# Kernel optimization log

Hardware: AMD Instinct MI355X
Metric: run time of the kernel (lower is better)

## Reference

```python
import jax, jax.numpy as jnp
import numpy as np

N, E, G = 4096, 16384, 128   # nodes, edges, graphs
IN, H, ED = 64, 64, 16       # in_dim, hidden, edge_dim


def _lin(key, fan_in, fan_out):
    return jax.random.normal(key, (fan_in, fan_out), dtype=jnp.float32) * (fan_in ** -0.5)


def setup_inputs() -> dict:
    key = jax.random.key(0)
    ks = jax.random.split(key, 32)
    inp = {
        "x": jax.random.normal(ks[0], (N, IN), dtype=jnp.float32),
        "edge_index": jax.random.randint(ks[1], (2, E), 0, N, dtype=jnp.int32),
        "edge_attr": jax.random.normal(ks[2], (E, ED), dtype=jnp.float32),
        "batch": jnp.sort(jax.random.randint(ks[3], (N,), 0, G, dtype=jnp.int32)),
    }
    ki = 4
    dims = [(IN, H), (H, H), (H, H)]  # (in_channels, out_channels) per layer
    for l, (ic, oc) in enumerate(dims):
        hd = ic * oc  # edge-MLP width = hidden * in_channels
        inp[f"l{l}_w1"] = _lin(ks[ki], ED, hd); ki += 1
        inp[f"l{l}_b1"] = jnp.zeros((hd,), dtype=jnp.float32)
        inp[f"l{l}_w2"] = _lin(ks[ki], hd, hd); ki += 1
        inp[f"l{l}_b2"] = jnp.zeros((hd,), dtype=jnp.float32)
        inp[f"l{l}_root"] = _lin(ks[ki], ic, oc); ki += 1
        inp[f"l{l}_bias"] = jnp.zeros((oc,), dtype=jnp.float32)
    return inp


def _nnconv(x, src, dst, edge_attr, w1, b1, w2, b2, root, bias, ic, oc):
    # per-edge weight matrix Theta(e): [E, ic, oc]
    h = jax.nn.relu(edge_attr @ w1 + b1)
    theta = (h @ w2 + b2).reshape(-1, ic, oc)
    # gather source features, per-edge bmm, scatter-mean to target
    msg = jnp.einsum("ei,eio->eo", x[src], theta)
    agg = jax.ops.segment_sum(msg, dst, num_segments=N)
    cnt = jax.ops.segment_sum(jnp.ones((msg.shape[0],), msg.dtype), dst, num_segments=N)
    agg = agg / jnp.maximum(cnt, 1.0)[:, None]
    return agg + x @ root + bias


def reference(x, edge_index, edge_attr, batch,
              l0_w1, l0_b1, l0_w2, l0_b2, l0_root, l0_bias,
              l1_w1, l1_b1, l1_w2, l1_b2, l1_root, l1_bias,
              l2_w1, l2_b1, l2_w2, l2_b2, l2_root, l2_bias):
    src, dst = edge_index[0], edge_index[1]
    layers = [
        (l0_w1, l0_b1, l0_w2, l0_b2, l0_root, l0_bias, IN, H),
        (l1_w1, l1_b1, l1_w2, l1_b2, l1_root, l1_bias, H, H),
        (l2_w1, l2_b1, l2_w2, l2_b2, l2_root, l2_bias, H, H),
    ]
    h = x
    for (w1, b1, w2, b2, root, bias, ic, oc) in layers:
        h = jax.nn.relu(_nnconv(h, src, dst, edge_attr, w1, b1, w2, b2, root, bias, ic, oc))
        # dropout is identity in eval mode
    # global mean pool over graphs
    s = jax.ops.segment_sum(h, batch, num_segments=G)
    c = jax.ops.segment_sum(jnp.ones((N,), h.dtype), batch, num_segments=G)
    return s / jnp.maximum(c, 1.0)[:, None]
```

## Files before the change

kernel.cpp:

```cpp
#include <hip/hip_runtime.h>
#include <hip/hip_bf16.h>

#define NN 4096
#define EE 16384
#define GG 128
#define EDIM 16
#define HD 4096

#define NGROUPS 64
#define GK 8
#define KSUBS 64
#define MAXT 40
#define MAXSLOT (MAXT * 16)
#define MAXTW 5
#define SYHALF (64 * 64 * 8)
#define PANEL (8 * 64 * 64)

typedef __attribute__((ext_vector_type(8))) short short8;
typedef __attribute__((ext_vector_type(4))) float float4v;

static __device__ inline unsigned short f2b(float f) {
    unsigned u = __float_as_uint(f);
    unsigned r = u + 0x7fff + ((u >> 16) & 1);
    return (unsigned short)(r >> 16);
}

static __device__ inline unsigned pk2(float a, float b) {
    __hip_bfloat162 p = __float22bfloat162_rn(make_float2(a, b));
    return *(unsigned*)&p;
}

__global__ void hker(const float* __restrict__ ea, const float* __restrict__ w1,
                     const float* __restrict__ b1, unsigned short* __restrict__ hB) {
    __shared__ float sea[16 * 16];
    const int tid = threadIdx.x;
    const int j = blockIdx.x * 256 + tid;
    const int e0 = blockIdx.y * 16;
    float w[16];
#pragma unroll
    for (int k = 0; k < 16; ++k) w[k] = w1[k * HD + j];
    const float b = b1[j];
    sea[tid] = ea[e0 * EDIM + tid];
    __syncthreads();
#pragma unroll 4
    for (int el = 0; el < 16; ++el) {
        float a = b;
#pragma unroll
        for (int k = 0; k < 16; ++k) a += sea[el * 16 + k] * w[k];
        hB[(size_t)(e0 + el) * HD + j] = f2b(fmaxf(a, 0.f));
    }
}

__global__ void wperm(const float* __restrict__ w2, unsigned short* __restrict__ W2q) {
    __shared__ float t[64 * 65];
    const int k = blockIdx.x;
    const int tid = threadIdx.x;
    const int o = tid & 63, r4 = tid >> 6;
#pragma unroll
    for (int it = 0; it < 16; ++it) {
        int i = it * 4 + r4;
        t[i * 65 + o] = w2[(size_t)k * HD + i * 64 + o];
    }
    __syncthreads();
    const int o2 = tid >> 2, q = tid & 3;
    const int q2 = q >> 1;
    const int j0 = (o2 >> 4) * 2 + q2;
    const int lmm = o2 & 15;
    const int blk = k;
#pragma unroll
    for (int cc = 0; cc < 2; ++cc) {
        const int quad = (q & 1) * 2 + cc;
        const int ib = q * 16 + cc * 8;
        size_t base = ((size_t)(blk * 64 + quad * 16 + lmm)) * 64 + j0 * 8;
        unsigned b0 = pk2(t[(ib + 0) * 65 + o2], t[(ib + 1) * 65 + o2]);
        unsigned b1 = pk2(t[(ib + 2) * 65 + o2], t[(ib + 3) * 65 + o2]);
        unsigned b2_ = pk2(t[(ib + 4) * 65 + o2], t[(ib + 5) * 65 + o2]);
        unsigned b3 = pk2(t[(ib + 6) * 65 + o2], t[(ib + 7) * 65 + o2]);
        *(uint4*)(&W2q[base]) = make_uint4(b0, b1, b2_, b3);
    }
}

__global__ void count_edges(const int* __restrict__ src, const int* __restrict__ dst,
                            int* __restrict__ cnt_src, float* __restrict__ cnt_dst) {
    const int e = blockIdx.x * 256 + threadIdx.x;
    atomicAdd(&cnt_src[src[e]], 1);
    atomicAdd(&cnt_dst[dst[e]], 1.f);
}

__global__ void build_layout(const int* __restrict__ cnt_src, int* __restrict__ node_slot_base,
                             int* __restrict__ tile_cluster, int* __restrict__ group_ntiles) {
    const int g = threadIdx.x;
    int nt = 0;
    int slot = g * MAXSLOT;
    for (int c = 0; c < 16; ++c) {
        int d = 0;
        for (int j = 0; j < 4; ++j) {
            int n = g * 64 + c * 4 + j;
            node_slot_base[n] = slot + d;
            d += cnt_src[n];
        }
        int tcnt = (d + 15) >> 4;
        if (nt + tcnt > MAXT) tcnt = MAXT - nt;
        for (int j = 0; j < tcnt; ++j) tile_cluster[g * MAXT + nt + j] = c;
        nt += tcnt;
        slot += tcnt * 16;
    }
    group_ntiles[g] = nt;
}

__global__ void fill_slots(const int* __restrict__ src, const int* __restrict__ dst,
                           int* __restrict__ fill, const int* __restrict__ node_slot_base,
                           int* __restrict__ slot_info) {
    const int e = blockIdx.x * 256 + threadIdx.x;
    const int n = src[e];
    const int pos = atomicAdd(&fill[n], 1);
    const int s = node_slot_base[n] + pos;
    const int g = n >> 6;
    if (s < g * MAXSLOT + MAXSLOT)
        slot_info[s] = e | ((n & 3) << 14) | (dst[e] << 16);
}

__global__ void xb_ker(const float* __restrict__ xcur, const float* __restrict__ b2,
                       float* __restrict__ xb) {
    const int n = blockIdx.x * 4 + (threadIdx.x >> 6);
    const int o = threadIdx.x & 63;
    float a = 0.f;
#pragma unroll
    for (int i = 0; i < 64; ++i) a += xcur[n * 64 + i] * b2[i * 64 + o];
    xb[n * 64 + o] = a;
}

__global__ void b2scatter(const float* __restrict__ xb, const int* __restrict__ src,
                          const int* __restrict__ dst, float* __restrict__ agg) {
    const int e = blockIdx.x * 4 + (threadIdx.x >> 6);
    const int o = threadIdx.x & 63;
    atomicAdd(&agg[(size_t)dst[e] * 64 + o], xb[(size_t)src[e] * 64 + o]);
}

__global__ __launch_bounds__(512, 2)
void ygemm_msg(const float* __restrict__ xcur, const unsigned short* __restrict__ hB,
               const unsigned short* __restrict__ W2q, const int* __restrict__ slot_info,
               const int* __restrict__ tile_cluster, const int* __restrict__ group_ntiles,
               float* __restrict__ agg) {
    __shared__ __align__(16) unsigned short sA[64 * 72];
    __shared__ __align__(16) unsigned short sY[2 * SYHALF];

    const int bid = blockIdx.x;
    const int g = bid >> 3;
    const int kc = bid & 7;
    const int tid = threadIdx.x;
    const int lane = tid & 63, wave = tid >> 6;
    const int quad = lane >> 4, lm = lane & 15;

    {
        const int n = tid >> 3, ib = (tid & 7) * 8;
        const float* xp = xcur + (size_t)(g * 64 + n) * 64 + ib;
        uint4 w = make_uint4(pk2(xp[0], xp[1]), pk2(xp[2], xp[3]),
                             pk2(xp[4], xp[5]), pk2(xp[6], xp[7]));
        *(uint4*)(&sA[n * 72 + ib]) = w;
    }

    const int ntiles = group_ntiles[g];
    int infoR[MAXTW], voff[MAXTW], rbase[MAXTW];
    unsigned shl5[MAXTW];
#pragma unroll
    for (int ai = 0; ai < MAXTW; ++ai) {
        const int ti = wave + ai * 8;
        const int info = (ti < ntiles) ? slot_info[g * MAXSLOT + ti * 16 + lm] : -1;
        const int tc   = (ti < ntiles) ? tile_cluster[g * MAXT + ti] : 0;
        infoR[ai] = info;
        voff[ai]  = ((info >= 0) ? (info & 0x3FFF) : EE) * HD + quad * 2;
        rbase[ai] = lm * 512 + (((tc * 4 + quad) ^ (lm & 7)) << 3);
        shl5[ai]  = (unsigned)(((info >> 14) & 3) * 16);
    }

    float4v acc2[MAXTW][4];
#pragma unroll
    for (int a = 0; a < MAXTW; ++a)
#pragma unroll
        for (int t = 0; t < 4; ++t) {
            acc2[a][t][0] = 0.f; acc2[a][t][1] = 0.f;
            acc2[a][t][2] = 0.f; acc2[a][t][3] = 0.f;
        }

    const int qg = wave >> 1, half = wave & 1;
    const int wb = lm * 512 + (((quad * 4 + qg) ^ (lm & 7)) << 3) + half * 4;
    __syncthreads();

    short8 af[4][2];
#pragma unroll
    for (int s = 0; s < 4; ++s)
#pragma unroll
        for (int q2 = 0; q2 < 2; ++q2)
            af[s][q2] = *(const short8*)(&sA[(s * 16 + lm) * 72 + q2 * 32 + quad * 8]);

    const float4v z4 = {0.f, 0.f, 0.f, 0.f};

    const unsigned short* wp  = W2q + ((size_t)(kc * KSUBS * 8 + wave) * 64 + lane) * 64;
    const unsigned short* hbk = hB + kc * KSUBS * 8;

    short8 BF[4][2];
#pragma unroll
    for (int tt = 0; tt < 4; ++tt) {
        BF[tt][0] = *(const short8*)(wp + (tt * 2 + 0) * 8);
        BF[tt][1] = *(const short8*)(wp + (tt * 2 + 1) * 8);
    }
    wp += PANEL;
    unsigned hdA[MAXTW], hdB[MAXTW];
#pragma unroll
    for (int ai = 0; ai < MAXTW; ++ai) {
        hdA[ai] = *(const unsigned*)(hbk + voff[ai]);
        hdB[ai] = *(const unsigned*)(hbk + 8 + voff[ai]);
    }

    int hoff = 16;

    auto subody = [&](unsigned (&HDc)[MAXTW], unsigned short* __restrict__ sYp) {
#pragma unroll
        for (int s = 0; s < 4; ++s) {
            float4v a1[4];
#pragma unroll
            for (int tt = 0; tt < 4; ++tt)
                a1[tt] = __builtin_amdgcn_mfma_f32_16x16x32_bf16(af[s][0], BF[tt][0], z4, 0, 0, 0);
#pragma unroll
            for (int tt = 0; tt < 4; ++tt)
                a1[tt] = __builtin_amdgcn_mfma_f32_16x16x32_bf16(af[s][1], BF[tt][1], a1[tt], 0, 0, 0);
#pragma unroll
            for (int tt = 0; tt < 4; ++tt) {
                uint2 v;
                v.x = pk2(a1[tt][0], a1[tt][1]);
                v.y = pk2(a1[tt][2], a1[tt][3]);
                *(uint2*)(&sYp[wb + s * 128 + tt * 8192]) = v;
            }
        }

        asm volatile("s_waitcnt lgkmcnt(0)" ::: "memory");
        __builtin_amdgcn_s_barrier();

#pragma unroll
        for (int tt = 0; tt < 4; ++tt) {
            BF[tt][0] = *(const short8*)(wp + (tt * 2 + 0) * 8);
            BF[tt][1] = *(const short8*)(wp + (tt * 2 + 1) * 8);
        }
        wp += PANEL;

#pragma unroll
        for (int ai = 0; ai < MAXTW; ++ai) {
            if (wave + ai * 8 < ntiles) {
                const unsigned h0 = HDc[ai];
                unsigned long long A = (unsigned long long)(h0 & 0xffffu) << shl5[ai];
                unsigned long long B = (unsigned long long)(h0 >> 16) << shl5[ai];
                uint4 aw = make_uint4((unsigned)A, (unsigned)(A >> 32),
                                      (unsigned)B, (unsigned)(B >> 32));
                short8 a2 = *(short8*)&aw;
#pragma unroll
                for (int ot = 0; ot < 4; ++ot) {
                    short8 b2f = *(const short8*)(&sYp[rbase[ai] + ot * 8192]);
                    acc2[ai][ot] = __builtin_amdgcn_mfma_f32_16x16x32_bf16(a2, b2f, acc2[ai][ot], 0, 0, 0);
                }
            }
        }

#pragma unroll
        for (int ai = 0; ai < MAXTW; ++ai)
            HDc[ai] = *(const unsigned*)(hbk + hoff + voff[ai]);
        hoff = (hoff < 504) ? hoff + 8 : 504;
    };

    for (int su2 = 0; su2 < KSUBS; su2 += 2) {
        subody(hdA, sY);
        subody(hdB, sY + SYHALF);
    }

#pragma unroll
    for (int ai = 0; ai < MAXTW; ++ai) {
        const int ti = wave + ai * 8;
        if (ti < ntiles) {
#pragma unroll
            for (int r = 0; r < 4; ++r) {
                const int inf2 = __shfl(infoR[ai], quad * 4 + r, 64);
                if (inf2 >= 0) {
                    const int d = inf2 >> 16;
#pragma unroll
                    for (int ot = 0; ot < 4; ++ot)
                        atomicAdd(&agg[(size_t)d * 64 + ot * 16 + lm], acc2[ai][ot][r]);
                }
            }
        }
    }
}

__global__ void combine(const float* __restrict__ agg, const float* __restrict__ cnt,
                        const float* __restrict__ xcur, const float* __restrict__ root,
                        const float* __restrict__ bias, float* __restrict__ xn) {
    const int n = blockIdx.x * 4 + (threadIdx.x >> 6);
    const int o = threadIdx.x & 63;
    float a = agg[n * 64 + o] / fmaxf(cnt[n], 1.f);
    float r = bias[o];
#pragma unroll
    for (int i = 0; i < 64; ++i) r += xcur[n * 64 + i] * root[i * 64 + o];
    xn[n * 64 + o] = fmaxf(a + r, 0.f);
}

__global__ void pool_accum(const float* __restrict__ x3, const int* __restrict__ batch,
                           float* __restrict__ pool, float* __restrict__ pcnt) {
    const int n = blockIdx.x * 4 + (threadIdx.x >> 6);
    const int o = threadIdx.x & 63;
    const int gi = batch[n];
    atomicAdd(&pool[gi * 64 + o], x3[n * 64 + o]);
    if (o == 0) atomicAdd(&pcnt[gi], 1.f);
}

__global__ void pool_norm(const float* __restrict__ pool, const float* __restrict__ pcnt,
                          float* __restrict__ out) {
    const int idx = blockIdx.x * 256 + threadIdx.x;
    out[idx] = pool[idx] / fmaxf(pcnt[idx >> 6], 1.f);
}

extern "C" void kernel_launch(void* const* d_in, const int* in_sizes, int n_in,
                              void* d_out, int out_size, void* d_ws, size_t ws_size,
                              hipStream_t stream) {
    const float* x   = (const float*)d_in[0];
    const int*   ei  = (const int*)d_in[1];
    const float* ea  = (const float*)d_in[2];
    const int*   bat = (const int*)d_in[3];
    const int* srcp = ei;
    const int* dstp = ei + EE;

    char* ws = (char*)d_ws;
    size_t off = 0;
    unsigned short* hB  = (unsigned short*)(ws + off); off += (size_t)(EE + 1) * HD * 2;
    unsigned short* W2q = (unsigned short*)(ws + off); off += ((size_t)HD * HD + PANEL) * 2;
    int* slot_info      = (int*)(ws + off); off += (size_t)NGROUPS * MAXSLOT * 4;
    int* tile_cluster   = (int*)(ws + off); off += (size_t)NGROUPS * MAXT * 4;
    int* group_ntiles   = (int*)(ws + off); off += 1024;
    int* node_slot_base = (int*)(ws + off); off += (size_t)NN * 4;
    int* cnt_src        = (int*)(ws + off); off += (size_t)NN * 4;
    int* fillc          = (int*)(ws + off); off += (size_t)NN * 4;
    float* cnt_dst      = (float*)(ws + off); off += (size_t)NN * 4;
    float* agg  = (float*)(ws + off); off += (size_t)NN * 64 * 4;
    float* xb   = (float*)(ws + off); off += (size_t)NN * 64 * 4;
    float* xb0  = (float*)(ws + off); off += (size_t)NN * 64 * 4;
    float* xb1  = (float*)(ws + off); off += (size_t)NN * 64 * 4;
    float* pool = (float*)(ws + off); off += (size_t)GG * 64 * 4;
    float* pcnt = (float*)(ws + off); off += (size_t)GG * 4;

    hipMemsetAsync(slot_info, 0xFF, (size_t)NGROUPS * MAXSLOT * 4, stream);
    hipMemsetAsync(cnt_src, 0, (size_t)NN * 4 * 3, stream);
    hipMemsetAsync(hB + (size_t)EE * HD, 0, (size_t)HD * 2, stream);
    count_edges<<<EE / 256, 256, 0, stream>>>(srcp, dstp, cnt_src, cnt_dst);
    build_layout<<<1, 64, 0, stream>>>(cnt_src, node_slot_base, tile_cluster, group_ntiles);
    fill_slots<<<EE / 256, 256, 0, stream>>>(srcp, dstp, fillc, node_slot_base, slot_info);

    const float* xcur = x;
    float* xbufs[2] = {xb0, xb1};

    for (int l = 0; l < 3; ++l) {
        const float* w1   = (const float*)d_in[4 + 6 * l + 0];
        const float* b1   = (const float*)d_in[4 + 6 * l + 1];
        const float* w2   = (const float*)d_in[4 + 6 * l + 2];
        const float* b2   = (const float*)d_in[4 + 6 * l + 3];
        const float* root = (const float*)d_in[4 + 6 * l + 4];
        const float* bias = (const float*)d_in[4 + 6 * l + 5];

        wperm<<<HD, 256, 0, stream>>>(w2, W2q);
        hker<<<dim3(HD / 256, EE / 16), 256, 0, stream>>>(ea, w1, b1, hB);
        xb_ker<<<NN / 4, 256, 0, stream>>>(xcur, b2, xb);
        hipMemsetAsync(agg, 0, (size_t)NN * 64 * 4, stream);
        b2scatter<<<EE / 4, 256, 0, stream>>>(xb, srcp, dstp, agg);
        ygemm_msg<<<NGROUPS * GK, 512, 0, stream>>>(xcur, hB, W2q, slot_info,
                                                    tile_cluster, group_ntiles, agg);
        float* xn = xbufs[l & 1];
        combine<<<NN / 4, 256, 0, stream>>>(agg, cnt_dst, xcur, root, bias, xn);
        xcur = xn;
    }
    hipMemsetAsync(pool, 0, (size_t)GG * 64 * 4 + (size_t)GG * 4, stream);
    pool_accum<<<NN / 4, 256, 0, stream>>>(xcur, bat, pool, pcnt);
    pool_norm<<<GG * 64 / 256, 256, 0, stream>>>(pool, pcnt, (float*)d_out);
}
```

Measured before the change: 1.621 ms.

## Double ygemm_msg block to 1024 threads, splitting Y-tile and edge-tile work across waves

The message GEMM kernel now runs 16 waves per block instead of 8. Each wave pair splits the first-stage Y computation in half (two output tiles instead of four), and the edge tiles are spread over 16 waves, so each wave holds at most 3 tiles. Fewer registers per wave should allow more waves in flight to hide memory and LDS latency. The cost is higher barrier participation per block, and launch bounds of 1024x4 may force register limits or spills.

```diff
diff --git a/kernel.cpp b/kernel.cpp
--- a/kernel.cpp
+++ b/kernel.cpp
@@ -12,7 +12,7 @@
 #define KSUBS 64
 #define MAXT 40
 #define MAXSLOT (MAXT * 16)
-#define MAXTW 5
+#define MAXTW 3
 #define SYHALF (64 * 64 * 8)
 #define PANEL (8 * 64 * 64)
 
@@ -137,7 +137,7 @@
     atomicAdd(&agg[(size_t)dst[e] * 64 + o], xb[(size_t)src[e] * 64 + o]);
 }
 
-__global__ __launch_bounds__(512, 2)
+__global__ __launch_bounds__(1024, 4)
 void ygemm_msg(const float* __restrict__ xcur, const unsigned short* __restrict__ hB,
                const unsigned short* __restrict__ W2q, const int* __restrict__ slot_info,
                const int* __restrict__ tile_cluster, const int* __restrict__ group_ntiles,
@@ -151,13 +151,14 @@
     const int tid = threadIdx.x;
     const int lane = tid & 63, wave = tid >> 6;
     const int quad = lane >> 4, lm = lane & 15;
+    const int kk = wave >> 1, sh = wave & 1;
+    const int qg = kk >> 1, half = kk & 1;
 
     {
-        const int n = tid >> 3, ib = (tid & 7) * 8;
+        const int n = tid >> 4, ib = (tid & 15) * 4;
         const float* xp = xcur + (size_t)(g * 64 + n) * 64 + ib;
-        uint4 w = make_uint4(pk2(xp[0], xp[1]), pk2(xp[2], xp[3]),
-                             pk2(xp[4], xp[5]), pk2(xp[6], xp[7]));
-        *(uint4*)(&sA[n * 72 + ib]) = w;
+        uint2 w = make_uint2(pk2(xp[0], xp[1]), pk2(xp[2], xp[3]));
+        *(uint2*)(&sA[n * 72 + ib]) = w;
     }
 
     const int ntiles = group_ntiles[g];
@@ -165,7 +166,7 @@
     unsigned shl5[MAXTW];
 #pragma unroll
     for (int ai = 0; ai < MAXTW; ++ai) {
-        const int ti = wave + ai * 8;
+        const int ti = wave + ai * 16;
         const int info = (ti < ntiles) ? slot_info[g * MAXSLOT + ti * 16 + lm] : -1;
         const int tc   = (ti < ntiles) ? tile_cluster[g * MAXT + ti] : 0;
         infoR[ai] = info;
@@ -183,8 +184,8 @@
             acc2[a][t][2] = 0.f; acc2[a][t][3] = 0.f;
         }
 
-    const int qg = wave >> 1, half = wave & 1;
-    const int wb = lm * 512 + (((quad * 4 + qg) ^ (lm & 7)) << 3) + half * 4;
+    const int wb = lm * 512 + (((quad * 4 + qg) ^ (lm & 7)) << 3) + half * 4
+                 + sh * 16384;
     __syncthreads();
 
     short8 af[4][2];
@@ -196,14 +197,14 @@
 
     const float4v z4 = {0.f, 0.f, 0.f, 0.f};
 
-    const unsigned short* wp  = W2q + ((size_t)(kc * KSUBS * 8 + wave) * 64 + lane) * 64;
+    const unsigned short* wp  = W2q + ((size_t)(kc * KSUBS * 8 + kk) * 64 + lane) * 64 + sh * 32;
     const unsigned short* hbk = hB + kc * KSUBS * 8;
 
-    short8 BF[4][2];
-#pragma unroll
-    for (int tt = 0; tt < 4; ++tt) {
-        BF[tt][0] = *(const short8*)(wp + (tt * 2 + 0) * 8);
-        BF[tt][1] = *(const short8*)(wp + (tt * 2 + 1) * 8);
+    short8 BF[2][2];
+#pragma unroll
+    for (int t2 = 0; t2 < 2; ++t2) {
+        BF[t2][0] = *(const short8*)(wp + (t2 * 2 + 0) * 8);
+        BF[t2][1] = *(const short8*)(wp + (t2 * 2 + 1) * 8);
     }
     wp += PANEL;
     unsigned hdA[MAXTW], hdB[MAXTW];
@@ -218,19 +219,19 @@
     auto subody = [&](unsigned (&HDc)[MAXTW], unsigned short* __restrict__ sYp) {
 #pragma unroll
         for (int s = 0; s < 4; ++s) {
-            float4v a1[4];
-#pragma unroll
-            for (int tt = 0; tt < 4; ++tt)
-                a1[tt] = __builtin_amdgcn_mfma_f32_16x16x32_bf16(af[s][0], BF[tt][0], z4, 0, 0, 0);
-#pragma unroll
-            for (int tt = 0; tt < 4; ++tt)
-                a1[tt] = __builtin_amdgcn_mfma_f32_16x16x32_bf16(af[s][1], BF[tt][1], a1[tt], 0, 0, 0);
-#pragma unroll
-            for (int tt = 0; tt < 4; ++tt) {
+            float4v a1[2];
+#pragma unroll
+            for (int t2 = 0; t2 < 2; ++t2)
+                a1[t2] = __builtin_amdgcn_mfma_f32_16x16x32_bf16(af[s][0], BF[t2][0], z4, 0, 0, 0);
+#pragma unroll
+            for (int t2 = 0; t2 < 2; ++t2)
+                a1[t2] = __builtin_amdgcn_mfma_f32_16x16x32_bf16(af[s][1], BF[t2][1], a1[t2], 0, 0, 0);
+#pragma unroll
+            for (int t2 = 0; t2 < 2; ++t2) {
                 uint2 v;
-                v.x = pk2(a1[tt][0], a1[tt][1]);
-                v.y = pk2(a1[tt][2], a1[tt][3]);
-                *(uint2*)(&sYp[wb + s * 128 + tt * 8192]) = v;
+                v.x = pk2(a1[t2][0], a1[t2][1]);
+                v.y = pk2(a1[t2][2], a1[t2][3]);
+                *(uint2*)(&sYp[wb + s * 128 + t2 * 8192]) = v;
             }
         }
 
@@ -238,15 +239,15 @@
         __builtin_amdgcn_s_barrier();
 
 #pragma unroll
-        for (int tt = 0; tt < 4; ++tt) {
-            BF[tt][0] = *(const short8*)(wp + (tt * 2 + 0) * 8);
-            BF[tt][1] = *(const short8*)(wp + (tt * 2 + 1) * 8);
+        for (int t2 = 0; t2 < 2; ++t2) {
+            BF[t2][0] = *(const short8*)(wp + (t2 * 2 + 0) * 8);
+            BF[t2][1] = *(const short8*)(wp + (t2 * 2 + 1) * 8);
         }
         wp += PANEL;
 
 #pragma unroll
         for (int ai = 0; ai < MAXTW; ++ai) {
-            if (wave + ai * 8 < ntiles) {
+            if (wave + ai * 16 < ntiles) {
                 const unsigned h0 = HDc[ai];
                 unsigned long long A = (unsigned long long)(h0 & 0xffffu) << shl5[ai];
                 unsigned long long B = (unsigned long long)(h0 >> 16) << shl5[ai];
@@ -274,7 +275,7 @@
 
 #pragma unroll
     for (int ai = 0; ai < MAXTW; ++ai) {
-        const int ti = wave + ai * 8;
+        const int ti = wave + ai * 16;
         if (ti < ntiles) {
 #pragma unroll
             for (int r = 0; r < 4; ++r) {
@@ -368,8 +369,8 @@
         xb_ker<<<NN / 4, 256, 0, stream>>>(xcur, b2, xb);
         hipMemsetAsync(agg, 0, (size_t)NN * 64 * 4, stream);
         b2scatter<<<EE / 4, 256, 0, stream>>>(xb, srcp, dstp, agg);
-        ygemm_msg<<<NGROUPS * GK, 512, 0, stream>>>(xcur, hB, W2q, slot_info,
-                                                    tile_cluster, group_ntiles, agg);
+        ygemm_msg<<<NGROUPS * GK, 1024, 0, stream>>>(xcur, hB, W2q, slot_info,
+                                                     tile_cluster, group_ntiles, agg);
         float* xn = xbufs[l & 1];
         combine<<<NN / 4, 256, 0, stream>>>(agg, cnt_dst, xcur, root, bias, xn);
         xcur = xn;
```

After: 1.684 ms. +3.9%, slower.

## Switch edge-message MFMA to 32x32x16 tiles with 32-edge tiles

Applied to the files above, without the earlier changes.

The per-edge message stage now uses 32x32x16 bf16 MFMA instructions on 32-edge tiles instead of 16x16x32 on 16-edge tiles. The slot layout, tile counts, hB column permutation, per-lane h loads (now uint2) and the atomic scatter indexing are reworked to match. The goal is fewer MFMA issues and LDS reads per edge, and fewer tiles per wave, which lowers register pressure. In exchange, clusters with few edges waste more padding in 32-slot tiles, and MAXT=30 caps slot capacity differently, which could drop edges if a group overflows.

```diff
diff --git a/kernel.cpp b/kernel.cpp
--- a/kernel.cpp
+++ b/kernel.cpp
@@ -10,14 +10,15 @@
 #define NGROUPS 64
 #define GK 8
 #define KSUBS 64
-#define MAXT 40
-#define MAXSLOT (MAXT * 16)
-#define MAXTW 5
+#define MAXT 30
+#define MAXSLOT (MAXT * 32)
+#define MAXTW 4
 #define SYHALF (64 * 64 * 8)
 #define PANEL (8 * 64 * 64)
 
 typedef __attribute__((ext_vector_type(8))) short short8;
 typedef __attribute__((ext_vector_type(4))) float float4v;
+typedef __attribute__((ext_vector_type(16))) float float16v;
 
 static __device__ inline unsigned short f2b(float f) {
     unsigned u = __float_as_uint(f);
@@ -42,12 +43,13 @@
     const float b = b1[j];
     sea[tid] = ea[e0 * EDIM + tid];
     __syncthreads();
+    const int js = (j & ~7) | (j & 1) | ((j & 2) << 1) | ((j & 4) >> 1);
 #pragma unroll 4
     for (int el = 0; el < 16; ++el) {
         float a = b;
 #pragma unroll
         for (int k = 0; k < 16; ++k) a += sea[el * 16 + k] * w[k];
-        hB[(size_t)(e0 + el) * HD + j] = f2b(fmaxf(a, 0.f));
+        hB[(size_t)(e0 + el) * HD + js] = f2b(fmaxf(a, 0.f));
     }
 }
 
@@ -99,11 +101,11 @@
             node_slot_base[n] = slot + d;
             d += cnt_src[n];
         }
-        int tcnt = (d + 15) >> 4;
+        int tcnt = (d + 31) >> 5;
         if (nt + tcnt > MAXT) tcnt = MAXT - nt;
         for (int j = 0; j < tcnt; ++j) tile_cluster[g * MAXT + nt + j] = c;
         nt += tcnt;
-        slot += tcnt * 16;
+        slot += tcnt * 32;
     }
     group_ntiles[g] = nt;
 }
@@ -151,6 +153,7 @@
     const int tid = threadIdx.x;
     const int lane = tid & 63, wave = tid >> 6;
     const int quad = lane >> 4, lm = lane & 15;
+    const int o5 = lane & 31, hh = lane >> 5;
 
     {
         const int n = tid >> 3, ib = (tid & 7) * 8;
@@ -161,27 +164,27 @@
     }
 
     const int ntiles = group_ntiles[g];
-    int infoR[MAXTW], voff[MAXTW], rbase[MAXTW];
+    int infoR[MAXTW], voff[MAXTW], rb0[MAXTW], rb1[MAXTW];
     unsigned shl5[MAXTW];
 #pragma unroll
     for (int ai = 0; ai < MAXTW; ++ai) {
         const int ti = wave + ai * 8;
-        const int info = (ti < ntiles) ? slot_info[g * MAXSLOT + ti * 16 + lm] : -1;
+        const int info = (ti < ntiles) ? slot_info[g * MAXSLOT + ti * 32 + o5] : -1;
         const int tc   = (ti < ntiles) ? tile_cluster[g * MAXT + ti] : 0;
         infoR[ai] = info;
-        voff[ai]  = ((info >= 0) ? (info & 0x3FFF) : EE) * HD + quad * 2;
-        rbase[ai] = lm * 512 + (((tc * 4 + quad) ^ (lm & 7)) << 3);
+        voff[ai]  = ((info >= 0) ? (info & 0x3FFF) : EE) * HD + hh * 4;
+        rb0[ai] = o5 * 512 + (((tc * 4 + hh)     ^ (o5 & 7)) << 3);
+        rb1[ai] = o5 * 512 + (((tc * 4 + 2 + hh) ^ (o5 & 7)) << 3);
         shl5[ai]  = (unsigned)(((info >> 14) & 3) * 16);
     }
 
-    float4v acc2[MAXTW][4];
+    float16v acc2[MAXTW][2];
 #pragma unroll
     for (int a = 0; a < MAXTW; ++a)
 #pragma unroll
-        for (int t = 0; t < 4; ++t) {
-            acc2[a][t][0] = 0.f; acc2[a][t][1] = 0.f;
-            acc2[a][t][2] = 0.f; acc2[a][t][3] = 0.f;
-        }
+        for (int t = 0; t < 2; ++t)
+#pragma unroll
+            for (int r = 0; r < 16; ++r) acc2[a][t][r] = 0.f;
 
     const int qg = wave >> 1, half = wave & 1;
     const int wb = lm * 512 + (((quad * 4 + qg) ^ (lm & 7)) << 3) + half * 4;
@@ -206,16 +209,16 @@
         BF[tt][1] = *(const short8*)(wp + (tt * 2 + 1) * 8);
     }
     wp += PANEL;
-    unsigned hdA[MAXTW], hdB[MAXTW];
+    uint2 hdA[MAXTW], hdB[MAXTW];
 #pragma unroll
     for (int ai = 0; ai < MAXTW; ++ai) {
-        hdA[ai] = *(const unsigned*)(hbk + voff[ai]);
-        hdB[ai] = *(const unsigned*)(hbk + 8 + voff[ai]);
+        hdA[ai] = *(const uint2*)(hbk + voff[ai]);
+        hdB[ai] = *(const uint2*)(hbk + 8 + voff[ai]);
     }
 
     int hoff = 16;
 
-    auto subody = [&](unsigned (&HDc)[MAXTW], unsigned short* __restrict__ sYp) {
+    auto subody = [&](uint2 (&HDc)[MAXTW], unsigned short* __restrict__ sYp) {
 #pragma unroll
         for (int s = 0; s < 4; ++s) {
             float4v a1[4];
@@ -247,23 +250,35 @@
 #pragma unroll
         for (int ai = 0; ai < MAXTW; ++ai) {
             if (wave + ai * 8 < ntiles) {
-                const unsigned h0 = HDc[ai];
-                unsigned long long A = (unsigned long long)(h0 & 0xffffu) << shl5[ai];
-                unsigned long long B = (unsigned long long)(h0 >> 16) << shl5[ai];
-                uint4 aw = make_uint4((unsigned)A, (unsigned)(A >> 32),
-                                      (unsigned)B, (unsigned)(B >> 32));
-                short8 a2 = *(short8*)&aw;
-#pragma unroll
-                for (int ot = 0; ot < 4; ++ot) {
-                    short8 b2f = *(const short8*)(&sYp[rbase[ai] + ot * 8192]);
-                    acc2[ai][ot] = __builtin_amdgcn_mfma_f32_16x16x32_bf16(a2, b2f, acc2[ai][ot], 0, 0, 0);
+                const uint2 hg = HDc[ai];
+                {
+                    unsigned long long A = (unsigned long long)(hg.x & 0xffffu) << shl5[ai];
+                    unsigned long long B = (unsigned long long)(hg.x >> 16) << shl5[ai];
+                    uint4 aw = make_uint4((unsigned)A, (unsigned)(A >> 32),
+                                          (unsigned)B, (unsigned)(B >> 32));
+                    short8 a2 = *(short8*)&aw;
+                    short8 b0 = *(const short8*)(&sYp[rb0[ai]]);
+                    acc2[ai][0] = __builtin_amdgcn_mfma_f32_32x32x16_bf16(a2, b0, acc2[ai][0], 0, 0, 0);
+                    short8 b1 = *(const short8*)(&sYp[rb0[ai] + 16384]);
+                    acc2[ai][1] = __builtin_amdgcn_mfma_f32_32x32x16_bf16(a2, b1, acc2[ai][1], 0, 0, 0);
+                }
+                {
+                    unsigned long long A = (unsigned long long)(hg.y & 0xffffu) << shl5[ai];
+                    unsigned long long B = (unsigned long long)(hg.y >> 16) << shl5[ai];
+                    uint4 aw = make_uint4((unsigned)A, (unsigned)(A >> 32),
+                                          (unsigned)B, (unsigned)(B >> 32));
+                    short8 a2 = *(short8*)&aw;
+                    short8 b0 = *(const short8*)(&sYp[rb1[ai]]);
+                    acc2[ai][0] = __builtin_amdgcn_mfma_f32_32x32x16_bf16(a2, b0, acc2[ai][0], 0, 0, 0);
+                    short8 b1 = *(const short8*)(&sYp[rb1[ai] + 16384]);
+                    acc2[ai][1] = __builtin_amdgcn_mfma_f32_32x32x16_bf16(a2, b1, acc2[ai][1], 0, 0, 0);
                 }
             }
         }
 
 #pragma unroll
         for (int ai = 0; ai < MAXTW; ++ai)
-            HDc[ai] = *(const unsigned*)(hbk + hoff + voff[ai]);
+            HDc[ai] = *(const uint2*)(hbk + hoff + voff[ai]);
         hoff = (hoff < 504) ? hoff + 8 : 504;
     };
 
@@ -277,13 +292,13 @@
         const int ti = wave + ai * 8;
         if (ti < ntiles) {
 #pragma unroll
-            for (int r = 0; r < 4; ++r) {
-                const int inf2 = __shfl(infoR[ai], quad * 4 + r, 64);
+            for (int r = 0; r < 16; ++r) {
+                const int slot = (r & 3) + 8 * (r >> 2) + 4 * hh;
+                const int inf2 = __shfl(infoR[ai], slot, 64);
                 if (inf2 >= 0) {
                     const int d = inf2 >> 16;
-#pragma unroll
-                    for (int ot = 0; ot < 4; ++ot)
-                        atomicAdd(&agg[(size_t)d * 64 + ot * 16 + lm], acc2[ai][ot][r]);
+                    atomicAdd(&agg[(size_t)d * 64 + o5],      acc2[ai][0][r]);
+                    atomicAdd(&agg[(size_t)d * 64 + 32 + o5], acc2[ai][1][r]);
                 }
             }
         }
```

Result: faster. 1.587 ms (-2.1%).
